# Optimization experiments

Measured on AMD Instinct MI355X. Metric: run time of the kernel, lower is better.

## Reference

```python
import jax, jax.numpy as jnp
import numpy as np

# Adjacent1d: locally-connected 1D op with per-output-position unshared weights.
# out[b, oc, os] = sum_{ic, k} x[b, ic, start(os)+k] * W[ic, k, oc, os] + bias[oc, os]
# where start(os) = floor(os * in_s / out_s). With in_s = out_s * kernel_size the
# windows tile the input exactly (matches the assert in_s/kernel_size <= out_s).

B, IN_C, IN_S = 4, 64, 16384
OUT_C, OUT_S = 64, 4096
K = 4


def setup_inputs() -> dict:
    key = jax.random.key(0)
    k1, k2, k3 = jax.random.split(key, 3)
    x = jax.random.normal(k1, (B, IN_C, IN_S), dtype=jnp.float32)
    weights = jax.random.normal(k2, (IN_C, K, OUT_C, OUT_S), dtype=jnp.float32) * 0.05
    bias = jax.random.normal(k3, (OUT_C, OUT_S), dtype=jnp.float32) * 0.05
    return {"x": x, "weights": weights, "bias": bias}


def reference(x, weights, bias):
    in_s = x.shape[-1]
    out_s = weights.shape[-1]
    k = weights.shape[1]
    # window start per output position (proportional mapping)
    starts = (jnp.arange(out_s) * in_s) // out_s          # [out_s]
    idx = starts[:, None] + jnp.arange(k)[None, :]        # [out_s, K]
    idx = jnp.minimum(idx, in_s - 1)                      # safety clamp (no-op when in_s = out_s*K)
    gathered = x[:, :, idx]                               # [B, in_c, out_s, K]
    # contract over input channels and kernel taps with per-position weights
    out = jnp.einsum('bisk,ikos->bos', gathered, weights) # [B, out_c, out_s]
    return out + bias[None, :, :]
```

## Files before the change

### kernel.cpp

```cpp
#include <hip/hip_runtime.h>


#define IN_C_  64
#define OUT_S_LOG2 12

__global__ __launch_bounds__(256) void adj1d_kernel(
    const float* __restrict__ x, const float* __restrict__ w,
    const float* __restrict__ bias, float* __restrict__ out) {

  int bid = blockIdx.x;
  int wgid = (bid & 7) * 64 + (bid >> 3);
  int og = wgid & 31;
  int st = wgid >> 5;
  int s  = (st << 8) + threadIdx.x;
  int o0 = og << 1;

  float acc00 = 0.f, acc01 = 0.f, acc02 = 0.f, acc03 = 0.f;
  float acc10 = 0.f, acc11 = 0.f, acc12 = 0.f, acc13 = 0.f;

  const float4* __restrict__ xv = reinterpret_cast<const float4*>(x);
  const float* __restrict__ wp0 = w + (o0 << OUT_S_LOG2) + s;

  #pragma unroll 2
  for (int i = 0; i < IN_C_; ++i) {
    float xa[4][4];
    *reinterpret_cast<float4*>(xa[0]) = xv[((0 * IN_C_ + i) << 12) + s];
    *reinterpret_cast<float4*>(xa[1]) = xv[((1 * IN_C_ + i) << 12) + s];
    *reinterpret_cast<float4*>(xa[2]) = xv[((2 * IN_C_ + i) << 12) + s];
    *reinterpret_cast<float4*>(xa[3]) = xv[((3 * IN_C_ + i) << 12) + s];
    #pragma unroll
    for (int k = 0; k < 4; ++k) {
      const float* wp = wp0 + (size_t)(i * 4 + k) * 262144;
      float wa = wp[0];
      float wb = wp[4096];
      acc00 = fmaf(xa[0][k], wa, acc00);
      acc01 = fmaf(xa[1][k], wa, acc01);
      acc02 = fmaf(xa[2][k], wa, acc02);
      acc03 = fmaf(xa[3][k], wa, acc03);
      acc10 = fmaf(xa[0][k], wb, acc10);
      acc11 = fmaf(xa[1][k], wb, acc11);
      acc12 = fmaf(xa[2][k], wb, acc12);
      acc13 = fmaf(xa[3][k], wb, acc13);
    }
  }

  float bA = bias[(o0 << OUT_S_LOG2) + s];
  float bB = bias[((o0 + 1) << OUT_S_LOG2) + s];

  out[((0 * 64 + o0) << OUT_S_LOG2) + s]     = acc00 + bA;
  out[((1 * 64 + o0) << OUT_S_LOG2) + s]     = acc01 + bA;
  out[((2 * 64 + o0) << OUT_S_LOG2) + s]     = acc02 + bA;
  out[((3 * 64 + o0) << OUT_S_LOG2) + s]     = acc03 + bA;
  out[((0 * 64 + o0 + 1) << OUT_S_LOG2) + s] = acc10 + bB;
  out[((1 * 64 + o0 + 1) << OUT_S_LOG2) + s] = acc11 + bB;
  out[((2 * 64 + o0 + 1) << OUT_S_LOG2) + s] = acc12 + bB;
  out[((3 * 64 + o0 + 1) << OUT_S_LOG2) + s] = acc13 + bB;
}

extern "C" void kernel_launch(void* const* d_in, const int* in_sizes, int n_in,
                              void* d_out, int out_size, void* d_ws, size_t ws_size,
                              hipStream_t stream) {
  const float* x    = (const float*)d_in[0];
  const float* w    = (const float*)d_in[1];
  const float* bias = (const float*)d_in[2];
  float* out = (float*)d_out;

  adj1d_kernel<<<512, 256, 0, stream>>>(x, w, bias, out);
}
```

Measured before the change: 63.26 us.

## Split input-channel reduction across two workgroups with atomic accumulation

Splits the 64-input-channel reduction into two halves handled by separate workgroups, doubling the grid from 512 to 1024 blocks so more waves hide memory latency on the weight stream. A separate kernel first writes the broadcast bias into the output, and the main kernel then atomically adds its partial sums. This adds a second launch, an extra output write and read-modify-write atomics, and makes the float summation order nondeterministic.

```diff
diff --git a/kernel.cpp b/kernel.cpp
--- a/kernel.cpp
+++ b/kernel.cpp
@@ -1,17 +1,24 @@
 #include <hip/hip_runtime.h>
 
 
-#define IN_C_  64
 #define OUT_S_LOG2 12
 
-__global__ __launch_bounds__(256) void adj1d_kernel(
+__global__ __launch_bounds__(256) void bias_init_kernel(
+    const float* __restrict__ bias, float* __restrict__ out) {
+  int t = blockIdx.x * 256 + threadIdx.x;
+  float4 bv = reinterpret_cast<const float4*>(bias)[t & 65535];
+  reinterpret_cast<float4*>(out)[t] = bv;
+}
+
+__global__ __launch_bounds__(256) void adj1d_acc_kernel(
     const float* __restrict__ x, const float* __restrict__ w,
-    const float* __restrict__ bias, float* __restrict__ out) {
+    float* __restrict__ out) {
 
   int bid = blockIdx.x;
-  int wgid = (bid & 7) * 64 + (bid >> 3);
-  int og = wgid & 31;
-  int st = wgid >> 5;
+  int wgid = (bid & 7) * 128 + (bid >> 3);
+  int ih = wgid & 1;
+  int og = (wgid >> 1) & 31;
+  int st = wgid >> 6;
   int s  = (st << 8) + threadIdx.x;
   int o0 = og << 1;
 
@@ -19,18 +26,21 @@
   float acc10 = 0.f, acc11 = 0.f, acc12 = 0.f, acc13 = 0.f;
 
   const float4* __restrict__ xv = reinterpret_cast<const float4*>(x);
-  const float* __restrict__ wp0 = w + (o0 << OUT_S_LOG2) + s;
+  const float* __restrict__ wp0 =
+      w + (size_t)ih * 32 * 4 * 262144 + (o0 << OUT_S_LOG2) + s;
+  int ibase = ih << 5;
 
   #pragma unroll 2
-  for (int i = 0; i < IN_C_; ++i) {
+  for (int ii = 0; ii < 32; ++ii) {
+    int i = ibase + ii;
     float xa[4][4];
-    *reinterpret_cast<float4*>(xa[0]) = xv[((0 * IN_C_ + i) << 12) + s];
-    *reinterpret_cast<float4*>(xa[1]) = xv[((1 * IN_C_ + i) << 12) + s];
-    *reinterpret_cast<float4*>(xa[2]) = xv[((2 * IN_C_ + i) << 12) + s];
-    *reinterpret_cast<float4*>(xa[3]) = xv[((3 * IN_C_ + i) << 12) + s];
+    *reinterpret_cast<float4*>(xa[0]) = xv[((0 * 64 + i) << 12) + s];
+    *reinterpret_cast<float4*>(xa[1]) = xv[((1 * 64 + i) << 12) + s];
+    *reinterpret_cast<float4*>(xa[2]) = xv[((2 * 64 + i) << 12) + s];
+    *reinterpret_cast<float4*>(xa[3]) = xv[((3 * 64 + i) << 12) + s];
     #pragma unroll
     for (int k = 0; k < 4; ++k) {
-      const float* wp = wp0 + (size_t)(i * 4 + k) * 262144;
+      const float* wp = wp0 + (size_t)(ii * 4 + k) * 262144;
       float wa = wp[0];
       float wb = wp[4096];
       acc00 = fmaf(xa[0][k], wa, acc00);
@@ -44,17 +54,14 @@
     }
   }
 
-  float bA = bias[(o0 << OUT_S_LOG2) + s];
-  float bB = bias[((o0 + 1) << OUT_S_LOG2) + s];
-
-  out[((0 * 64 + o0) << OUT_S_LOG2) + s]     = acc00 + bA;
-  out[((1 * 64 + o0) << OUT_S_LOG2) + s]     = acc01 + bA;
-  out[((2 * 64 + o0) << OUT_S_LOG2) + s]     = acc02 + bA;
-  out[((3 * 64 + o0) << OUT_S_LOG2) + s]     = acc03 + bA;
-  out[((0 * 64 + o0 + 1) << OUT_S_LOG2) + s] = acc10 + bB;
-  out[((1 * 64 + o0 + 1) << OUT_S_LOG2) + s] = acc11 + bB;
-  out[((2 * 64 + o0 + 1) << OUT_S_LOG2) + s] = acc12 + bB;
-  out[((3 * 64 + o0 + 1) << OUT_S_LOG2) + s] = acc13 + bB;
+  unsafeAtomicAdd(&out[((0 * 64 + o0) << OUT_S_LOG2) + s],     acc00);
+  unsafeAtomicAdd(&out[((1 * 64 + o0) << OUT_S_LOG2) + s],     acc01);
+  unsafeAtomicAdd(&out[((2 * 64 + o0) << OUT_S_LOG2) + s],     acc02);
+  unsafeAtomicAdd(&out[((3 * 64 + o0) << OUT_S_LOG2) + s],     acc03);
+  unsafeAtomicAdd(&out[((0 * 64 + o0 + 1) << OUT_S_LOG2) + s], acc10);
+  unsafeAtomicAdd(&out[((1 * 64 + o0 + 1) << OUT_S_LOG2) + s], acc11);
+  unsafeAtomicAdd(&out[((2 * 64 + o0 + 1) << OUT_S_LOG2) + s], acc12);
+  unsafeAtomicAdd(&out[((3 * 64 + o0 + 1) << OUT_S_LOG2) + s], acc13);
 }
 
 extern "C" void kernel_launch(void* const* d_in, const int* in_sizes, int n_in,
@@ -65,5 +72,6 @@
   const float* bias = (const float*)d_in[2];
   float* out = (float*)d_out;
 
-  adj1d_kernel<<<512, 256, 0, stream>>>(x, w, bias, out);
+  bias_init_kernel<<<1024, 256, 0, stream>>>(bias, out);
+  adj1d_acc_kernel<<<1024, 256, 0, stream>>>(x, w, out);
 }
```

Result: slower. 67.49 us (+6.7%).
